# Kernel tuning notes

Measured on AMD Instinct MI355X. Metric: run time of the kernel, lower is better.

The kernel has to match this reference:

```python
import jax, jax.numpy as jnp
import numpy as np

S = 64.0   # arcface scale
M = 0.5    # arcface additive angular margin
EPS = 1e-07
B, D, C = 1024, 512, 100000


def setup_inputs() -> dict:
    key = jax.random.key(0)
    k1, k2, k3 = jax.random.split(key, 3)
    features = jax.random.normal(k1, (B, D), dtype=jnp.float32)
    # Linear(512, 100000, bias=False) weight, ~1/sqrt(512) init scale.
    W = jax.random.normal(k2, (C, D), dtype=jnp.float32) * 0.04
    y_true = jax.random.randint(k3, (B,), 0, C, dtype=jnp.int64)
    return {"features": features, "W": W, "y_true": y_true}


def reference(features, W, y_true):
    # L2-normalize features along dim=1 (torch F.normalize, eps=1e-12).
    norm = jnp.maximum(jnp.linalg.norm(features, axis=1, keepdims=True), 1e-12)
    xn = features / norm
    # NOTE: the original module's weight-normalization loop is a no-op
    # (rebinds a local), so W is used unnormalized — faithful to the source.
    wf = xn @ W.T                                   # [B, C] cosine-like logits
    tgt = wf[jnp.arange(B), y_true]                  # true-class logit per row
    # arcface: s * cos(acos(clamp(t)) + m)
    numerator = S * jnp.cos(jnp.arccos(jnp.clip(tgt, -1.0 + EPS, 1.0 - EPS)) + M)
    # exp-sum over all classes except the true one (mask instead of python-loop concat)
    not_true = jnp.arange(C)[None, :] != y_true[:, None]   # [B, C]
    excl_sum = jnp.sum(jnp.where(not_true, jnp.exp(S * wf), 0.0), axis=1)
    denominator = jnp.exp(numerator) + excl_sum
    L = numerator - jnp.log(denominator)
    return -jnp.mean(L)
```

## Files before the change

kernel.cpp:

```cpp
#include <hip/hip_runtime.h>
#include <math.h>

#define BATCH 1024
#define DIM   512
#define NCLS  100000
#define SCALE_S 64.0f
#define MARGIN  0.5f
#define EPS_REF 1e-7f
#define SEXP 92.332482616893656878f

#define NSLAB 64
#define NBLK  1563
#define CHUNK 16
#define NCHUNK_WAVE 16
#define NRSCOPY 8

typedef __attribute__((ext_vector_type(4))) float floatx4;
typedef __attribute__((ext_vector_type(2))) long  longx2;

#if __has_builtin(__builtin_amdgcn_exp2f)
#define EXP2(x) __builtin_amdgcn_exp2f(x)
#else
#define EXP2(x) exp2f(x)
#endif

__device__ __forceinline__ float red16(float v) {
    int x;
    x = __builtin_amdgcn_update_dpp(0, __builtin_bit_cast(int, v), 0x128, 0xf, 0xf, true);
    v += __builtin_bit_cast(float, x);
    x = __builtin_amdgcn_update_dpp(0, __builtin_bit_cast(int, v), 0x124, 0xf, 0xf, true);
    v += __builtin_bit_cast(float, x);
    x = __builtin_amdgcn_update_dpp(0, __builtin_bit_cast(int, v), 0x4E, 0xf, 0xf, true);
    v += __builtin_bit_cast(float, x);
    x = __builtin_amdgcn_update_dpp(0, __builtin_bit_cast(int, v), 0xB1, 0xf, 0xf, true);
    v += __builtin_bit_cast(float, x);
    return v;
}

__global__ __launch_bounds__(256)
void k_prep(const float* __restrict__ features,
            const float* __restrict__ W,
            const int* __restrict__ y,
            unsigned char* __restrict__ xf8,
            float* __restrict__ rowsum,
            float* __restrict__ tgt) {
    const int row = blockIdx.x;
    const int t = threadIdx.x;
    const int lane = t & 63;
    const int wave = t >> 6;
    __shared__ float redS[4], redD[4];

    const float2 v  = *(const float2*)(features + (size_t)row * DIM + t * 2);
    const float2 wv = *(const float2*)(W + (size_t)y[row] * DIM + t * 2);
    float ss = v.x * v.x + v.y * v.y;
    float dd = v.x * wv.x + v.y * wv.y;
    #pragma unroll
    for (int m = 32; m >= 1; m >>= 1) { ss += __shfl_xor(ss, m); dd += __shfl_xor(dd, m); }
    if (lane == 0) { redS[wave] = ss; redD[wave] = dd; }
    __syncthreads();
    const float tot  = redS[0] + redS[1] + redS[2] + redS[3];
    const float dtot = redD[0] + redD[1] + redD[2] + redD[3];
    const float nrm = fmaxf(sqrtf(tot), 1e-12f);
    const float sc = SEXP / nrm;

    int pk = __builtin_amdgcn_cvt_pk_fp8_f32(v.x * sc, v.y * sc, 0, false);
    const int k0 = t * 2;
    const int off = ((k0 & 31) >> 3) * 128 + (k0 >> 5) * 8 + (k0 & 7);
    *(unsigned short*)(xf8 + (size_t)row * DIM + off) = (unsigned short)(pk & 0xFFFF);

    if (t < NRSCOPY) rowsum[t * BATCH + row] = 0.0f;
    if (t == 0) tgt[row] = dtot / nrm;
}


#define STEPJ(Ab, jj) {                                                        \
    const longx2 q0 = *(const longx2*)(&Ws[0 * 8192 + bbase + (((jj) ^ swb) << 4)]); \
    const longx2 q1 = *(const longx2*)(&Ws[1 * 8192 + bbase + (((jj) ^ swb) << 4)]); \
    const longx2 q2 = *(const longx2*)(&Ws[2 * 8192 + bbase + (((jj) ^ swb) << 4)]); \
    const longx2 q3 = *(const longx2*)(&Ws[3 * 8192 + bbase + (((jj) ^ swb) << 4)]); \
    const long a0 = Ab[jj][0];                                                 \
    const long a1 = Ab[jj][1];                                                 \
    acc0 = __builtin_amdgcn_mfma_f32_16x16x32_fp8_fp8(a0, q0[0], acc0, 0, 0, 0); \
    acc1 = __builtin_amdgcn_mfma_f32_16x16x32_fp8_fp8(a0, q1[0], acc1, 0, 0, 0); \
    acc2 = __builtin_amdgcn_mfma_f32_16x16x32_fp8_fp8(a0, q2[0], acc2, 0, 0, 0); \
    acc3 = __builtin_amdgcn_mfma_f32_16x16x32_fp8_fp8(a0, q3[0], acc3, 0, 0, 0); \
    acc0 = __builtin_amdgcn_mfma_f32_16x16x32_fp8_fp8(a1, q0[1], acc0, 0, 0, 0); \
    acc1 = __builtin_amdgcn_mfma_f32_16x16x32_fp8_fp8(a1, q1[1], acc1, 0, 0, 0); \
    acc2 = __builtin_amdgcn_mfma_f32_16x16x32_fp8_fp8(a1, q2[1], acc2, 0, 0, 0); \
    acc3 = __builtin_amdgcn_mfma_f32_16x16x32_fp8_fp8(a1, q3[1], acc3, 0, 0, 0); }

#define LA(Ab, c) { const unsigned char* p_ = abase + (size_t)(c) * (CHUNK * DIM); \
    Ab[0] = *(const longx2*)(p_ +  0); Ab[1] = *(const longx2*)(p_ + 16);      \
    Ab[2] = *(const longx2*)(p_ + 32); Ab[3] = *(const longx2*)(p_ + 48);      \
    Ab[4] = *(const longx2*)(p_ + 64); Ab[5] = *(const longx2*)(p_ + 80);      \
    Ab[6] = *(const longx2*)(p_ + 96); Ab[7] = *(const longx2*)(p_ + 112); }

#define EPI(reg) { float p_;                                                   \
    if (full) { p_ = EXP2(acc0[reg]) + EXP2(acc1[reg])                         \
                   + EXP2(acc2[reg]) + EXP2(acc3[reg]); }                      \
    else { p_ = 0.f;                                                           \
        if (n0 +      l15 < NCLS) p_ += EXP2(acc0[reg]);                       \
        if (n0 + 16 + l15 < NCLS) p_ += EXP2(acc1[reg]);                       \
        if (n0 + 32 + l15 < NCLS) p_ += EXP2(acc2[reg]);                       \
        if (n0 + 48 + l15 < NCLS) p_ += EXP2(acc3[reg]); }                     \
    p_ = red16(p_);                                                            \
    if (l15 == 0) atomicAdd(&rs[rowb_ + (reg)], p_); }

#define COMPUTE(Ab, c) {                                                       \
    floatx4 acc0 = (floatx4){0.f,0.f,0.f,0.f};                                 \
    floatx4 acc1 = (floatx4){0.f,0.f,0.f,0.f};                                 \
    floatx4 acc2 = (floatx4){0.f,0.f,0.f,0.f};                                 \
    floatx4 acc3 = (floatx4){0.f,0.f,0.f,0.f};                                 \
    __builtin_amdgcn_s_setprio(1);                                             \
    STEPJ(Ab,0) STEPJ(Ab,1) STEPJ(Ab,2) STEPJ(Ab,3)                            \
    STEPJ(Ab,4) STEPJ(Ab,5) STEPJ(Ab,6) STEPJ(Ab,7)                            \
    __builtin_amdgcn_s_setprio(0);                                             \
    const int rowb_ = (wave * NCHUNK_WAVE + (c)) * CHUNK + quad * 4;           \
    EPI(0) EPI(1) EPI(2) EPI(3) }

__global__ __launch_bounds__(256, 2)
void k_gemm_fused(const float* __restrict__ W,
                  const unsigned char* __restrict__ xf8,
                  float* __restrict__ rowsum) {
    __shared__ __align__(16) unsigned char Ws[NSLAB * DIM];

    const int tid  = threadIdx.x;
    const int wave = tid >> 6;
    const int lane = tid & 63;
    const int quad = lane >> 4;
    const int l15  = lane & 15;
    const int n0   = blockIdx.x * NSLAB;
    float* rs = rowsum + (blockIdx.x & (NRSCOPY - 1)) * BATCH;

    const int bbase = l15 * 512 + quad * 128;
    const int swb   = l15 & 7;

    const unsigned char* abase =
        xf8 + (size_t)(wave * NCHUNK_WAVE * CHUNK + l15) * DIM + quad * 128;

    longx2 A0[8], A1[8];
    LA(A0, 0)

    #pragma unroll
    for (int j = 0; j < 8; ++j) {
        const int c   = j * 256 + tid;
        const int r   = c >> 5;
        const int rem = c & 31;
        const int jj  = rem >> 2;
        const int qd  = rem & 3;
        int rg = n0 + r; if (rg > NCLS - 1) rg = NCLS - 1;
        const float* src = W + (size_t)rg * DIM + jj * 64 + qd * 8;
        const float4 e0 = *(const float4*)(src);
        const float4 e1 = *(const float4*)(src + 4);
        const float4 o0 = *(const float4*)(src + 32);
        const float4 o1 = *(const float4*)(src + 36);
        int w0 = __builtin_amdgcn_cvt_pk_fp8_f32(e0.x, e0.y, 0, false);
        w0     = __builtin_amdgcn_cvt_pk_fp8_f32(e0.z, e0.w, w0, true);
        int w1 = __builtin_amdgcn_cvt_pk_fp8_f32(e1.x, e1.y, 0, false);
        w1     = __builtin_amdgcn_cvt_pk_fp8_f32(e1.z, e1.w, w1, true);
        int w2 = __builtin_amdgcn_cvt_pk_fp8_f32(o0.x, o0.y, 0, false);
        w2     = __builtin_amdgcn_cvt_pk_fp8_f32(o0.z, o0.w, w2, true);
        int w3 = __builtin_amdgcn_cvt_pk_fp8_f32(o1.x, o1.y, 0, false);
        w3     = __builtin_amdgcn_cvt_pk_fp8_f32(o1.z, o1.w, w3, true);
        *(int4*)(&Ws[r * 512 + ((qd * 8 + (jj ^ (r & 7))) << 4)]) =
            make_int4(w0, w1, w2, w3);
    }
    __syncthreads();

    const bool full = (n0 + NSLAB <= NCLS);

    #pragma unroll 1
    for (int c = 0; c < NCHUNK_WAVE; c += 2) {
        LA(A1, c + 1)
        COMPUTE(A0, c)
        const int cn = (c + 2 < NCHUNK_WAVE) ? c + 2 : 0;
        LA(A0, cn)
        COMPUTE(A1, c + 1)
    }
}

__global__ void k_finalize(const float* __restrict__ rowsum,
                           const float* __restrict__ tgt,
                           float* __restrict__ out) {
    const int tid = threadIdx.x;
    const int lane = tid & 63;
    const int wave = tid >> 6;
    __shared__ float red[4];

    float s = 0.f;
    #pragma unroll
    for (int i = 0; i < 4; ++i) {
        const int b = tid + i * 256;
        float rsum = 0.f;
        #pragma unroll
        for (int cp = 0; cp < NRSCOPY; ++cp) rsum += rowsum[cp * BATCH + b];
        const float traw = tgt[b];
        const float tc = fminf(fmaxf(traw, -1.0f + EPS_REF), 1.0f - EPS_REF);
        const float num = SCALE_S * cosf(acosf(tc) + MARGIN);
        const float excl = rsum - expf(SCALE_S * traw);
        const float denom = expf(num) + excl;
        s += num - logf(denom);
    }
    #pragma unroll
    for (int m = 32; m >= 1; m >>= 1) s += __shfl_xor(s, m);
    if (lane == 0) red[wave] = s;
    __syncthreads();
    if (tid == 0)
        out[0] = -(red[0] + red[1] + red[2] + red[3]) / (float)BATCH;
}

extern "C" void kernel_launch(void* const* d_in, const int* in_sizes, int n_in,
                              void* d_out, int out_size, void* d_ws, size_t ws_size,
                              hipStream_t stream) {
    const float* features = (const float*)d_in[0];
    const float* W        = (const float*)d_in[1];
    const int*   y        = (const int*)d_in[2];
    float* out = (float*)d_out;

    const size_t XF8_BYTES = (size_t)BATCH * DIM;
    const size_t RS_BYTES  = (size_t)NRSCOPY * BATCH * sizeof(float);
    char* ws = (char*)d_ws;
    unsigned char* xf8 = (unsigned char*)ws;
    float* rowsum = (float*)(ws + XF8_BYTES);
    float* tgt    = (float*)(ws + XF8_BYTES + RS_BYTES);

    k_prep<<<BATCH, 256, 0, stream>>>(features, W, y, xf8, rowsum, tgt);
    k_gemm_fused<<<NBLK, 256, 0, stream>>>(W, xf8, rowsum);
    k_finalize<<<1, 256, 0, stream>>>(rowsum, tgt, out);
}
```

Measured before the change: 380.7 us.

## Switch fused GEMM from 16x16x32 to 32x32x16 fp8 MFMA tiles

Replaces the 16x16x32 fp8 MFMA tiling with 32x32x16 MFMA. The feature and weight fp8 layouts in global and shared memory are reorganised to match, along with the swizzle and the epilogue row mapping. Each wave now handles 32-row chunks, so it issues fewer LDS reads and gets more A/B reuse per MFMA. In exchange it needs more registers (16-wide accumulators and 16-entry A buffers), which may hurt occupancy at launch bounds of 2, and it issues more atomics per chunk in the epilogue.

```diff
diff --git a/kernel.cpp b/kernel.cpp
--- a/kernel.cpp
+++ b/kernel.cpp
@@ -11,12 +11,12 @@
 
 #define NSLAB 64
 #define NBLK  1563
-#define CHUNK 16
-#define NCHUNK_WAVE 16
+#define CHUNK 32
+#define NCHUNK_WAVE 8
 #define NRSCOPY 8
 
-typedef __attribute__((ext_vector_type(4))) float floatx4;
-typedef __attribute__((ext_vector_type(2))) long  longx2;
+typedef __attribute__((ext_vector_type(16))) float floatx16;
+typedef __attribute__((ext_vector_type(2)))  long  longx2;
 
 #if __has_builtin(__builtin_amdgcn_exp2f)
 #define EXP2(x) __builtin_amdgcn_exp2f(x)
@@ -65,7 +65,7 @@
 
     int pk = __builtin_amdgcn_cvt_pk_fp8_f32(v.x * sc, v.y * sc, 0, false);
     const int k0 = t * 2;
-    const int off = ((k0 & 31) >> 3) * 128 + (k0 >> 5) * 8 + (k0 & 7);
+    const int off = ((k0 >> 3) & 1) * 256 + (k0 >> 4) * 8 + (k0 & 7);
     *(unsigned short*)(xf8 + (size_t)row * DIM + off) = (unsigned short)(pk & 0xFFFF);
 
     if (t < NRSCOPY) rowsum[t * BATCH + row] = 0.0f;
@@ -73,50 +73,47 @@
 }
 
 
-#define STEPJ(Ab, jj) {                                                        \
-    const longx2 q0 = *(const longx2*)(&Ws[0 * 8192 + bbase + (((jj) ^ swb) << 4)]); \
-    const longx2 q1 = *(const longx2*)(&Ws[1 * 8192 + bbase + (((jj) ^ swb) << 4)]); \
-    const longx2 q2 = *(const longx2*)(&Ws[2 * 8192 + bbase + (((jj) ^ swb) << 4)]); \
-    const longx2 q3 = *(const longx2*)(&Ws[3 * 8192 + bbase + (((jj) ^ swb) << 4)]); \
-    const long a0 = Ab[jj][0];                                                 \
-    const long a1 = Ab[jj][1];                                                 \
-    acc0 = __builtin_amdgcn_mfma_f32_16x16x32_fp8_fp8(a0, q0[0], acc0, 0, 0, 0); \
-    acc1 = __builtin_amdgcn_mfma_f32_16x16x32_fp8_fp8(a0, q1[0], acc1, 0, 0, 0); \
-    acc2 = __builtin_amdgcn_mfma_f32_16x16x32_fp8_fp8(a0, q2[0], acc2, 0, 0, 0); \
-    acc3 = __builtin_amdgcn_mfma_f32_16x16x32_fp8_fp8(a0, q3[0], acc3, 0, 0, 0); \
-    acc0 = __builtin_amdgcn_mfma_f32_16x16x32_fp8_fp8(a1, q0[1], acc0, 0, 0, 0); \
-    acc1 = __builtin_amdgcn_mfma_f32_16x16x32_fp8_fp8(a1, q1[1], acc1, 0, 0, 0); \
-    acc2 = __builtin_amdgcn_mfma_f32_16x16x32_fp8_fp8(a1, q2[1], acc2, 0, 0, 0); \
-    acc3 = __builtin_amdgcn_mfma_f32_16x16x32_fp8_fp8(a1, q3[1], acc3, 0, 0, 0); }
-
-#define LA(Ab, c) { const unsigned char* p_ = abase + (size_t)(c) * (CHUNK * DIM); \
-    Ab[0] = *(const longx2*)(p_ +  0); Ab[1] = *(const longx2*)(p_ + 16);      \
-    Ab[2] = *(const longx2*)(p_ + 32); Ab[3] = *(const longx2*)(p_ + 48);      \
-    Ab[4] = *(const longx2*)(p_ + 64); Ab[5] = *(const longx2*)(p_ + 80);      \
-    Ab[6] = *(const longx2*)(p_ + 96); Ab[7] = *(const longx2*)(p_ + 112); }
+#define STEPJ(Af, jj) {                                                        \
+    const longx2 q0_ = *(const longx2*)(&Ws[        bb + (((jj) ^ swb) << 4)]); \
+    const longx2 q1_ = *(const longx2*)(&Ws[16384 + bb + (((jj) ^ swb) << 4)]); \
+    acc0 = __builtin_amdgcn_mfma_f32_32x32x16_fp8_fp8(Af[jj][0], q0_[0], acc0, 0, 0, 0); \
+    acc1 = __builtin_amdgcn_mfma_f32_32x32x16_fp8_fp8(Af[jj][0], q1_[0], acc1, 0, 0, 0); \
+    acc0 = __builtin_amdgcn_mfma_f32_32x32x16_fp8_fp8(Af[jj][1], q0_[1], acc0, 0, 0, 0); \
+    acc1 = __builtin_amdgcn_mfma_f32_32x32x16_fp8_fp8(Af[jj][1], q1_[1], acc1, 0, 0, 0); }
+
+#define LA16(Af, c) { const unsigned char* p_ = abase + (size_t)(c) * 16384;   \
+    Af[0]  = *(const longx2*)(p_ +   0); Af[1]  = *(const longx2*)(p_ +  16);  \
+    Af[2]  = *(const longx2*)(p_ +  32); Af[3]  = *(const longx2*)(p_ +  48);  \
+    Af[4]  = *(const longx2*)(p_ +  64); Af[5]  = *(const longx2*)(p_ +  80);  \
+    Af[6]  = *(const longx2*)(p_ +  96); Af[7]  = *(const longx2*)(p_ + 112);  \
+    Af[8]  = *(const longx2*)(p_ + 128); Af[9]  = *(const longx2*)(p_ + 144);  \
+    Af[10] = *(const longx2*)(p_ + 160); Af[11] = *(const longx2*)(p_ + 176);  \
+    Af[12] = *(const longx2*)(p_ + 192); Af[13] = *(const longx2*)(p_ + 208);  \
+    Af[14] = *(const longx2*)(p_ + 224); Af[15] = *(const longx2*)(p_ + 240); }
 
 #define EPI(reg) { float p_;                                                   \
-    if (full) { p_ = EXP2(acc0[reg]) + EXP2(acc1[reg])                         \
-                   + EXP2(acc2[reg]) + EXP2(acc3[reg]); }                      \
+    if (full) { p_ = EXP2(acc0[reg]) + EXP2(acc1[reg]); }                      \
     else { p_ = 0.f;                                                           \
-        if (n0 +      l15 < NCLS) p_ += EXP2(acc0[reg]);                       \
-        if (n0 + 16 + l15 < NCLS) p_ += EXP2(acc1[reg]);                       \
-        if (n0 + 32 + l15 < NCLS) p_ += EXP2(acc2[reg]);                       \
-        if (n0 + 48 + l15 < NCLS) p_ += EXP2(acc3[reg]); }                     \
+        if (n0 +      c31 < NCLS) p_ += EXP2(acc0[reg]);                       \
+        if (n0 + 32 + c31 < NCLS) p_ += EXP2(acc1[reg]); }                     \
     p_ = red16(p_);                                                            \
-    if (l15 == 0) atomicAdd(&rs[rowb_ + (reg)], p_); }
-
-#define COMPUTE(Ab, c) {                                                       \
-    floatx4 acc0 = (floatx4){0.f,0.f,0.f,0.f};                                 \
-    floatx4 acc1 = (floatx4){0.f,0.f,0.f,0.f};                                 \
-    floatx4 acc2 = (floatx4){0.f,0.f,0.f,0.f};                                 \
-    floatx4 acc3 = (floatx4){0.f,0.f,0.f,0.f};                                 \
+    if ((lane & 15) == 0)                                                      \
+        atomicAdd(&rs[crow_ + ((reg) & 3) + 8 * ((reg) >> 2) + 4 * hi], p_); }
+
+#define COMPUTE(Af, c) {                                                       \
+    floatx16 acc0 = {0.f,0.f,0.f,0.f,0.f,0.f,0.f,0.f,                          \
+                     0.f,0.f,0.f,0.f,0.f,0.f,0.f,0.f};                         \
+    floatx16 acc1 = {0.f,0.f,0.f,0.f,0.f,0.f,0.f,0.f,                          \
+                     0.f,0.f,0.f,0.f,0.f,0.f,0.f,0.f};                         \
     __builtin_amdgcn_s_setprio(1);                                             \
-    STEPJ(Ab,0) STEPJ(Ab,1) STEPJ(Ab,2) STEPJ(Ab,3)                            \
-    STEPJ(Ab,4) STEPJ(Ab,5) STEPJ(Ab,6) STEPJ(Ab,7)                            \
+    STEPJ(Af,0)  STEPJ(Af,1)  STEPJ(Af,2)  STEPJ(Af,3)                         \
+    STEPJ(Af,4)  STEPJ(Af,5)  STEPJ(Af,6)  STEPJ(Af,7)                         \
+    STEPJ(Af,8)  STEPJ(Af,9)  STEPJ(Af,10) STEPJ(Af,11)                        \
+    STEPJ(Af,12) STEPJ(Af,13) STEPJ(Af,14) STEPJ(Af,15)                        \
     __builtin_amdgcn_s_setprio(0);                                             \
-    const int rowb_ = (wave * NCHUNK_WAVE + (c)) * CHUNK + quad * 4;           \
-    EPI(0) EPI(1) EPI(2) EPI(3) }
+    const int crow_ = (wave * NCHUNK_WAVE + (c)) * CHUNK;                      \
+    EPI(0)  EPI(1)  EPI(2)  EPI(3)  EPI(4)  EPI(5)  EPI(6)  EPI(7)             \
+    EPI(8)  EPI(9)  EPI(10) EPI(11) EPI(12) EPI(13) EPI(14) EPI(15) }
 
 __global__ __launch_bounds__(256, 2)
 void k_gemm_fused(const float* __restrict__ W,
@@ -127,33 +124,33 @@
     const int tid  = threadIdx.x;
     const int wave = tid >> 6;
     const int lane = tid & 63;
-    const int quad = lane >> 4;
-    const int l15  = lane & 15;
+    const int c31  = lane & 31;
+    const int hi   = lane >> 5;
     const int n0   = blockIdx.x * NSLAB;
     float* rs = rowsum + (blockIdx.x & (NRSCOPY - 1)) * BATCH;
 
-    const int bbase = l15 * 512 + quad * 128;
-    const int swb   = l15 & 7;
+    const int bb  = c31 * 512 + hi * 256;
+    const int swb = c31 & 15;
 
     const unsigned char* abase =
-        xf8 + (size_t)(wave * NCHUNK_WAVE * CHUNK + l15) * DIM + quad * 128;
-
-    longx2 A0[8], A1[8];
-    LA(A0, 0)
+        xf8 + (size_t)(wave * NCHUNK_WAVE * CHUNK + c31) * DIM + hi * 256;
+
+    longx2 Aa[16], Ab[16];
+    LA16(Aa, 0)
 
     #pragma unroll
     for (int j = 0; j < 8; ++j) {
         const int c   = j * 256 + tid;
         const int r   = c >> 5;
-        const int rem = c & 31;
-        const int jj  = rem >> 2;
-        const int qd  = rem & 3;
+        const int c16 = c & 31;
+        const int jjw = c16 & 15;
+        const int hiw = c16 >> 4;
         int rg = n0 + r; if (rg > NCLS - 1) rg = NCLS - 1;
-        const float* src = W + (size_t)rg * DIM + jj * 64 + qd * 8;
+        const float* src = W + (size_t)rg * DIM + jjw * 32 + hiw * 8;
         const float4 e0 = *(const float4*)(src);
         const float4 e1 = *(const float4*)(src + 4);
-        const float4 o0 = *(const float4*)(src + 32);
-        const float4 o1 = *(const float4*)(src + 36);
+        const float4 o0 = *(const float4*)(src + 16);
+        const float4 o1 = *(const float4*)(src + 20);
         int w0 = __builtin_amdgcn_cvt_pk_fp8_f32(e0.x, e0.y, 0, false);
         w0     = __builtin_amdgcn_cvt_pk_fp8_f32(e0.z, e0.w, w0, true);
         int w1 = __builtin_amdgcn_cvt_pk_fp8_f32(e1.x, e1.y, 0, false);
@@ -162,7 +159,7 @@
         w2     = __builtin_amdgcn_cvt_pk_fp8_f32(o0.z, o0.w, w2, true);
         int w3 = __builtin_amdgcn_cvt_pk_fp8_f32(o1.x, o1.y, 0, false);
         w3     = __builtin_amdgcn_cvt_pk_fp8_f32(o1.z, o1.w, w3, true);
-        *(int4*)(&Ws[r * 512 + ((qd * 8 + (jj ^ (r & 7))) << 4)]) =
+        *(int4*)(&Ws[r * 512 + hiw * 256 + ((jjw ^ (r & 15)) << 4)]) =
             make_int4(w0, w1, w2, w3);
     }
     __syncthreads();
@@ -171,11 +168,10 @@
 
     #pragma unroll 1
     for (int c = 0; c < NCHUNK_WAVE; c += 2) {
-        LA(A1, c + 1)
-        COMPUTE(A0, c)
-        const int cn = (c + 2 < NCHUNK_WAVE) ? c + 2 : 0;
-        LA(A0, cn)
-        COMPUTE(A1, c + 1)
+        LA16(Ab, c + 1)
+        COMPUTE(Aa, c)
+        LA16(Aa, (c + 2) & 7)
+        COMPUTE(Ab, c + 1)
     }
 }
 
```

After: 625.3 us. +64.3%, slower.
